# Kernel tuning notes

Measured on AMD Instinct MI355X. Metric: run time of the kernel, lower is better.

## Reference

```python
import jax, jax.numpy as jnp
import numpy as np

IN_F = 4096
OUT_F = 8192
BLOCK = 16   # block_dim
KEEP = 8     # keep_k low-frequency modes kept per block
NLEV = 256   # n_levels


def dct_inv_basis(keep_k, n):
    # Orthonormal DCT-II synthesis basis, rows = kept frequencies k, cols = time index t.
    k = jnp.arange(keep_k, dtype=jnp.float32)[:, None]
    t = jnp.arange(n, dtype=jnp.float32)[None, :]
    B = jnp.cos(jnp.pi * (t + 0.5) * k / n) * jnp.sqrt(2.0 / n)
    scale = jnp.where(jnp.arange(keep_k) == 0, 1.0 / jnp.sqrt(2.0), 1.0)
    return B * scale[:, None]  # [keep_k, block_dim]


def setup_inputs() -> dict:
    key = jax.random.key(0)
    k1, k2, k3, k4, k5 = jax.random.split(key, 5)
    n_blocks = OUT_F * IN_F // BLOCK  # 2097152
    x = jax.random.normal(k1, (32, 8, IN_F), jnp.float32)
    idx = jax.random.randint(k2, (n_blocks, KEEP), 0, NLEV, jnp.int32)
    c_min = jax.random.normal(k3, (KEEP,), jnp.float32)
    c_range = jax.random.uniform(k4, (KEEP,), jnp.float32) + 0.1
    bias = jax.random.normal(k5, (OUT_F,), jnp.float32)
    return {"x": x, "idx": idx, "c_min": c_min, "c_range": c_range, "bias": bias}


def reference(x, idx, c_min, c_range, bias):
    # Affine dequant of kept frequency codes: [n_blocks, keep_k]
    coeffs = idx.astype(jnp.float32) / (NLEV - 1) * c_range + c_min
    # Inverse DCT per block (high-frequency modes are implicitly zero)
    B = dct_inv_basis(KEEP, BLOCK)              # [keep_k, block_dim]
    W = (coeffs @ B).reshape(OUT_F, IN_F)       # dense dequantized weight
    return x @ W.T + bias
```

## Files before the change

kernel.cpp:

```cpp
#include <hip/hip_runtime.h>


typedef __attribute__((ext_vector_type(8))) short bf16x8;
typedef __attribute__((ext_vector_type(4))) float f32x4;

#define K_TOT   2048
#define N_TOT   8192
#define NT      32
#define NCHUNK  8
#define SPC     8
#define LDS_CH  16384

__device__ __forceinline__ unsigned short f2bf_rn(float f) {
    unsigned u = __float_as_uint(f);
    u += 0x7FFFu + ((u >> 16) & 1u);
    return (unsigned short)(u >> 16);
}
__device__ __forceinline__ unsigned pack2(int a, int b) {
    unsigned ua = __float_as_uint((float)a);
    unsigned ub = __float_as_uint((float)b);
    return __builtin_amdgcn_perm(ub, ua, 0x07060302u);
}

__device__ __forceinline__ void lds_barrier() {
    asm volatile("" ::: "memory");
    __builtin_amdgcn_s_waitcnt(0xC07F);
    __builtin_amdgcn_s_barrier();
    asm volatile("" ::: "memory");
}

__global__ __launch_bounds__(256) void prep_kernel(
    const float* __restrict__ x, const float* __restrict__ c_min,
    const float* __restrict__ c_range, unsigned short* __restrict__ Y2f,
    float* __restrict__ corr)
{
    __shared__ float Bk[8][16];
    __shared__ float scmin[8];
    __shared__ float ss[8];
    __shared__ float red[4];
    const int tid = threadIdx.x;
    const int m = blockIdx.x;
    if (tid < 128) {
        int k = tid >> 4, t = tid & 15;
        float v = cosf(3.14159265358979f * (t + 0.5f) * (float)k / 16.0f)
                  * 0.353553390593274f;
        if (k == 0) v *= 0.707106781186548f;
        Bk[k][t] = v;
    }
    if (tid < 8) {
        scmin[tid] = c_min[tid];
        ss[tid] = c_range[tid] * (1.0f / 255.0f);
    }
    __syncthreads();

    const float* xp = x + (long)m * 4096 + tid * 16;
    float xs[16];
#pragma unroll
    for (int q = 0; q < 4; ++q) {
        float4 v = *(const float4*)(xp + q * 4);
        xs[q * 4 + 0] = v.x; xs[q * 4 + 1] = v.y;
        xs[q * 4 + 2] = v.z; xs[q * 4 + 3] = v.w;
    }
    float partial = 0.0f;
    unsigned short yo[8];
#pragma unroll
    for (int k = 0; k < 8; ++k) {
        float y = 0.0f;
#pragma unroll
        for (int t = 0; t < 16; ++t) y += xs[t] * Bk[k][t];
        partial += y * scmin[k];
        yo[k] = f2bf_rn(y * ss[k]);
    }
    uint4 pk;
    pk.x = (unsigned)yo[0] | ((unsigned)yo[1] << 16);
    pk.y = (unsigned)yo[2] | ((unsigned)yo[3] << 16);
    pk.z = (unsigned)yo[4] | ((unsigned)yo[5] << 16);
    pk.w = (unsigned)yo[6] | ((unsigned)yo[7] << 16);
    {
        const int mg = m >> 4, fr = m & 15, kc = tid >> 2, fq = tid & 3;
        unsigned short* dst = Y2f + ((long)((mg * 64 + kc) * 64) + fq * 16 + fr) * 8;
        *(uint4*)dst = pk;
    }
#pragma unroll
    for (int off = 32; off > 0; off >>= 1)
        partial += __shfl_down(partial, off, 64);
    if ((tid & 63) == 0) red[tid >> 6] = partial;
    __syncthreads();
    if (tid == 0) corr[m] = red[0] + red[1] + red[2] + red[3];
}

__global__ __launch_bounds__(512, 2) void gemm_kernel(
    const unsigned short* __restrict__ Y2f, const int* __restrict__ idx,
    const float* __restrict__ bias, const float* __restrict__ corr,
    float* __restrict__ out)
{
    __shared__ char lds[NCHUNK * LDS_CH];
    __shared__ int flags[NCHUNK];

    const int tid  = threadIdx.x;
    const int wave = tid >> 6;
    const int lane = tid & 63;
    const int o0   = blockIdx.x * NT;

    if (tid < NCHUNK) flags[tid] = 0;

    if (wave >= 4) {
        const int p    = tid - 256;
        const int scol = p >> 3;
        const int sk8  = p & 7;
        const int* pBase = idx + (long)(o0 + scol) * K_TOT + sk8 * 4;

        int4 S[2][8];
#define PLOAD(slot, ch)                                                   \
        {                                                                 \
            _Pragma("unroll")                                             \
            for (int r = 0; r < 8; ++r)                                   \
                S[slot][r] = *(const int4*)(pBase + (ch) * 256 + r * 32); \
        }
        PLOAD(0, 0)
        PLOAD(1, 1)
        lds_barrier();

#pragma unroll
        for (int c = 0; c < NCHUNK; ++c) {
            char* buf = lds + c * LDS_CH;
#pragma unroll
            for (int r = 0; r < 8; ++r) {
                const int kq = sk8 + r * 8;
                uint2 w;
                w.x = pack2(S[c & 1][r].x, S[c & 1][r].y);
                w.y = pack2(S[c & 1][r].z, S[c & 1][r].w);
                *(uint2*)(buf + scol * 512 + (((kq >> 1) ^ scol) * 16)
                          + (kq & 1) * 8) = w;
            }
            __builtin_amdgcn_s_waitcnt(0xC07F);
            if (lane == 0)
                __hip_atomic_fetch_add(&flags[c], 1, __ATOMIC_RELEASE,
                                       __HIP_MEMORY_SCOPE_WORKGROUP);
            const int nc = (c + 2 < NCHUNK) ? (c + 2) : (NCHUNK - 1);
            PLOAD(c & 1, nc)
        }
#undef PLOAD
    } else {
        const int fr = lane & 15;
        const int fq = lane >> 4;
        const bf16x8* aF = (const bf16x8*)Y2f + (long)(wave * 4) * 64 * 64 + lane;

        f32x4 acc[4][2];
#pragma unroll
        for (int mt = 0; mt < 4; ++mt)
#pragma unroll
            for (int g = 0; g < 2; ++g)
                acc[mt][g] = (f32x4){0.f, 0.f, 0.f, 0.f};

        bf16x8 a[4][4];
#pragma unroll
        for (int d = 0; d < 4; ++d)
#pragma unroll
            for (int mt = 0; mt < 4; ++mt)
                a[d][mt] = aF[mt * 4096 + d * 64];

        lds_barrier();

#define BREAD(buf, s, g)                                                  \
    (*(const bf16x8*)((buf) + (g * 16 + fr) * 512 +                       \
                      ((((s) * 4 + fq) ^ (g * 16 + fr)) * 16)))

        for (int c = 0; c < NCHUNK; ++c) {
            while (__hip_atomic_load(&flags[c], __ATOMIC_ACQUIRE,
                                     __HIP_MEMORY_SCOPE_WORKGROUP) < 4)
                __builtin_amdgcn_s_sleep(1);
            const char* buf = lds + c * LDS_CH;
#pragma unroll
            for (int s = 0; s < SPC; ++s) {
                bf16x8 b0 = BREAD(buf, s, 0);
                bf16x8 b1 = BREAD(buf, s, 1);
#pragma unroll
                for (int mt = 0; mt < 4; ++mt) {
                    acc[mt][0] = __builtin_amdgcn_mfma_f32_16x16x32_bf16(
                        a[s & 3][mt], b0, acc[mt][0], 0, 0, 0);
                    acc[mt][1] = __builtin_amdgcn_mfma_f32_16x16x32_bf16(
                        a[s & 3][mt], b1, acc[mt][1], 0, 0, 0);
                }
                {
                    const long nks = (long)c * SPC + s + 4;
#pragma unroll
                    for (int mt = 0; mt < 4; ++mt)
                        a[s & 3][mt] = aF[mt * 4096 + nks * 64];
                }
            }
        }
#undef BREAD

#pragma unroll
        for (int mt = 0; mt < 4; ++mt) {
#pragma unroll
            for (int g = 0; g < 2; ++g) {
                const int col = o0 + g * 16 + fr;
                const float bv = bias[col];
                const int row0 = (wave * 4 + mt) * 16 + fq * 4;
#pragma unroll
                for (int r = 0; r < 4; ++r)
                    out[(long)(row0 + r) * N_TOT + col] =
                        acc[mt][g][r] + bv + corr[row0 + r];
            }
        }
    }
}

extern "C" void kernel_launch(void* const* d_in, const int* in_sizes, int n_in,
                              void* d_out, int out_size, void* d_ws, size_t ws_size,
                              hipStream_t stream) {
    const float* x       = (const float*)d_in[0];
    const int*   idx     = (const int*)d_in[1];
    const float* c_min   = (const float*)d_in[2];
    const float* c_range = (const float*)d_in[3];
    const float* bias    = (const float*)d_in[4];
    float* out = (float*)d_out;

    unsigned short* Y2f = (unsigned short*)d_ws;
    float* corr = (float*)((char*)d_ws + (size_t)256 * K_TOT * 2);

    prep_kernel<<<256, 256, 0, stream>>>(x, c_min, c_range, Y2f, corr);
    gemm_kernel<<<256, 512, 0, stream>>>(Y2f, idx, bias, corr, out);
}
```

Before: 130.8 us.

## Replace atomic chunk flags with per-wave flags, widen producer stores, deepen A prefetch

Producer waves now each own 8 columns and write 16-byte packed LDS stores instead of 8-byte ones. Each producer wave sets its own per-chunk flag with a volatile store, replacing the atomic counter. Consumers spin on the four flags with plain volatile loads and no sleep. The consumer's A-operand register prefetch goes from 4 k-steps to 8 and the chunk loop is fully unrolled, with the prefetch index wrapped mod 64. The aim is to cut atomic and synchronisation overhead and hide global load latency better, at the cost of more registers (risking occupancy under launch bounds 512,2), busy-spinning, and weaker memory ordering than release/acquire atomics.

```diff
diff --git a/kernel.cpp b/kernel.cpp
--- a/kernel.cpp
+++ b/kernel.cpp
@@ -95,27 +95,31 @@
     float* __restrict__ out)
 {
     __shared__ char lds[NCHUNK * LDS_CH];
-    __shared__ int flags[NCHUNK];
+    __shared__ int flags[NCHUNK][4];
 
     const int tid  = threadIdx.x;
     const int wave = tid >> 6;
     const int lane = tid & 63;
     const int o0   = blockIdx.x * NT;
 
-    if (tid < NCHUNK) flags[tid] = 0;
+    if (tid < NCHUNK * 4) flags[tid >> 2][tid & 3] = 0;
 
     if (wave >= 4) {
-        const int p    = tid - 256;
-        const int scol = p >> 3;
-        const int sk8  = p & 7;
-        const int* pBase = idx + (long)(o0 + scol) * K_TOT + sk8 * 4;
-
-        int4 S[2][8];
+        const int pw   = wave - 4;
+        const int col  = pw * 8 + (lane >> 3);
+        const int pr0  = lane & 7;
+        const int* pBase = idx + (long)(o0 + col) * K_TOT + pr0 * 8;
+        char* cBase = lds + col * 512;
+
+        int4 S[2][4][2];
 #define PLOAD(slot, ch)                                                   \
         {                                                                 \
             _Pragma("unroll")                                             \
-            for (int r = 0; r < 8; ++r)                                   \
-                S[slot][r] = *(const int4*)(pBase + (ch) * 256 + r * 32); \
+            for (int r = 0; r < 4; ++r) {                                 \
+                const int* p = pBase + (ch) * 256 + r * 64;               \
+                S[slot][r][0] = *(const int4*)p;                          \
+                S[slot][r][1] = *(const int4*)(p + 4);                    \
+            }                                                             \
         }
         PLOAD(0, 0)
         PLOAD(1, 1)
@@ -123,20 +127,17 @@
 
 #pragma unroll
         for (int c = 0; c < NCHUNK; ++c) {
-            char* buf = lds + c * LDS_CH;
-#pragma unroll
-            for (int r = 0; r < 8; ++r) {
-                const int kq = sk8 + r * 8;
-                uint2 w;
-                w.x = pack2(S[c & 1][r].x, S[c & 1][r].y);
-                w.y = pack2(S[c & 1][r].z, S[c & 1][r].w);
-                *(uint2*)(buf + scol * 512 + (((kq >> 1) ^ scol) * 16)
-                          + (kq & 1) * 8) = w;
-            }
-            __builtin_amdgcn_s_waitcnt(0xC07F);
-            if (lane == 0)
-                __hip_atomic_fetch_add(&flags[c], 1, __ATOMIC_RELEASE,
-                                       __HIP_MEMORY_SCOPE_WORKGROUP);
+#pragma unroll
+            for (int r = 0; r < 4; ++r) {
+                uint4 w;
+                w.x = pack2(S[c & 1][r][0].x, S[c & 1][r][0].y);
+                w.y = pack2(S[c & 1][r][0].z, S[c & 1][r][0].w);
+                w.z = pack2(S[c & 1][r][1].x, S[c & 1][r][1].y);
+                w.w = pack2(S[c & 1][r][1].z, S[c & 1][r][1].w);
+                *(uint4*)(cBase + c * LDS_CH + (((pr0 + 8 * r) ^ col) * 16)) = w;
+            }
+            asm volatile("s_waitcnt lgkmcnt(0)" ::: "memory");
+            if (lane == 0) *(volatile int*)&flags[c][pw] = 1;
             const int nc = (c + 2 < NCHUNK) ? (c + 2) : (NCHUNK - 1);
             PLOAD(c & 1, nc)
         }
@@ -144,7 +145,7 @@
     } else {
         const int fr = lane & 15;
         const int fq = lane >> 4;
-        const bf16x8* aF = (const bf16x8*)Y2f + (long)(wave * 4) * 64 * 64 + lane;
+        const bf16x8* aF = (const bf16x8*)Y2f + (long)(wave * 4) * 4096 + lane;
 
         f32x4 acc[4][2];
 #pragma unroll
@@ -153,9 +154,9 @@
             for (int g = 0; g < 2; ++g)
                 acc[mt][g] = (f32x4){0.f, 0.f, 0.f, 0.f};
 
-        bf16x8 a[4][4];
-#pragma unroll
-        for (int d = 0; d < 4; ++d)
+        bf16x8 a[8][4];
+#pragma unroll
+        for (int d = 0; d < 8; ++d)
 #pragma unroll
             for (int mt = 0; mt < 4; ++mt)
                 a[d][mt] = aF[mt * 4096 + d * 64];
@@ -166,10 +167,16 @@
     (*(const bf16x8*)((buf) + (g * 16 + fr) * 512 +                       \
                       ((((s) * 4 + fq) ^ (g * 16 + fr)) * 16)))
 
+#pragma unroll
         for (int c = 0; c < NCHUNK; ++c) {
-            while (__hip_atomic_load(&flags[c], __ATOMIC_ACQUIRE,
-                                     __HIP_MEMORY_SCOPE_WORKGROUP) < 4)
-                __builtin_amdgcn_s_sleep(1);
+            for (;;) {
+                int f0 = *(volatile int*)&flags[c][0];
+                int f1 = *(volatile int*)&flags[c][1];
+                int f2 = *(volatile int*)&flags[c][2];
+                int f3 = *(volatile int*)&flags[c][3];
+                if (f0 & f1 & f2 & f3) break;
+            }
+            asm volatile("" ::: "memory");
             const char* buf = lds + c * LDS_CH;
 #pragma unroll
             for (int s = 0; s < SPC; ++s) {
@@ -178,15 +185,15 @@
 #pragma unroll
                 for (int mt = 0; mt < 4; ++mt) {
                     acc[mt][0] = __builtin_amdgcn_mfma_f32_16x16x32_bf16(
-                        a[s & 3][mt], b0, acc[mt][0], 0, 0, 0);
+                        a[s][mt], b0, acc[mt][0], 0, 0, 0);
                     acc[mt][1] = __builtin_amdgcn_mfma_f32_16x16x32_bf16(
-                        a[s & 3][mt], b1, acc[mt][1], 0, 0, 0);
+                        a[s][mt], b1, acc[mt][1], 0, 0, 0);
                 }
                 {
-                    const long nks = (long)c * SPC + s + 4;
+                    const int nks = (c * SPC + s + 8) & 63;
 #pragma unroll
                     for (int mt = 0; mt < 4; ++mt)
-                        a[s & 3][mt] = aF[mt * 4096 + nks * 64];
+                        a[s][mt] = aF[mt * 4096 + nks * 64];
                 }
             }
         }
```

Result: faster. 120.6 us (-7.8%).
